# Kernel optimization log

Hardware: AMD Instinct MI355X
Metric: run time of the kernel (lower is better)

The kernel has to match this reference:

```python
import jax, jax.numpy as jnp
import numpy as np

NUM_REGIONS = 64
K_NEIGHBORS = 5
REGION_LAMBDA = 0.02
SPATIAL_LAMBDA = 0.0005


def setup_inputs() -> dict:
    key = jax.random.key(0)
    k1, k2, k3 = jax.random.split(key, 3)
    B = 16384
    c_points = jax.random.normal(k1, (B, 3), dtype=jnp.float32)
    coords_std = jax.random.normal(k2, (B, 3), dtype=jnp.float32)
    region_ids = jax.random.randint(k3, (B,), 0, NUM_REGIONS, dtype=jnp.int32)
    return {"c_points": c_points, "coords_std": coords_std, "region_ids": region_ids}


def _region_loss(c_points, region_ids):
    # Equivalent to per-region pairwise dispersion via segment reductions:
    # 2 * sum||c - mean_r||^2 / (max(n_r*(n_r-1)/2, 1) * xdim), summed over regions.
    dtype = c_points.dtype
    xdim = jnp.asarray(c_points.shape[1], dtype)
    ones = jnp.ones(c_points.shape[0], dtype)
    counts = jax.ops.segment_sum(ones, region_ids, num_segments=NUM_REGIONS)          # [R]
    sums = jax.ops.segment_sum(c_points, region_ids, num_segments=NUM_REGIONS)        # [R,3]
    sqs = jax.ops.segment_sum(c_points * c_points, region_ids, num_segments=NUM_REGIONS)  # [R,3]
    safe_n = jnp.maximum(counts, 1.0)
    mean = sums / safe_n[:, None]
    sum_sq_centered = jnp.sum(sqs - counts[:, None] * mean * mean, axis=1)             # [R]
    n_pairs = counts * (counts - 1.0) * 0.5
    denom = jnp.maximum(n_pairs, 1.0) * xdim
    per_region = jnp.where(counts > 1.0, 2.0 * sum_sq_centered / denom, 0.0)
    return jnp.asarray(REGION_LAMBDA, dtype) * jnp.sum(per_region)


def _spatial_loss(c_points, coords_std):
    # Dense pairwise squared distances, exclude self, KNN gather, mean squared diff of cuts.
    dtype = c_points.dtype
    B = coords_std.shape[0]
    xdim = jnp.asarray(c_points.shape[1], dtype)
    c2 = jnp.sum(coords_std * coords_std, axis=1, keepdims=True)                       # [B,1]
    d2 = c2 - 2.0 * (coords_std @ coords_std.T) + c2.T                                 # [B,B]
    big = jnp.max(d2) + 1.0
    diag = jnp.arange(B)
    d2 = d2.at[diag, diag].set(big)
    _, idxs = jax.lax.top_k(-d2, K_NEIGHBORS)                                          # [B,k]
    c_nb = c_points[idxs]                                                              # [B,k,3]
    diffs = c_points[:, None, :] - c_nb
    sq = jnp.sum(diffs * diffs, axis=2)                                                # [B,k]
    loss = jnp.mean(jnp.mean(sq, axis=1))
    return jnp.asarray(SPATIAL_LAMBDA, dtype) * (loss / jnp.maximum(xdim, 1.0))


def reference(c_points, coords_std, region_ids):
    return _region_loss(c_points, region_ids) + _spatial_loss(c_points, coords_std)
```

## Files before the change

kernel.cpp:

```cpp
#include <hip/hip_runtime.h>
#include <stdint.h>

#define B_N    16384
#define NREG   64
#define KNB    5
#define SAMPLE 4096
#define NSUB   16
#define SUBLEN (SAMPLE / NSUB)
#define NCH    32
#define CHLEN  (B_N / NCH)
#define MRGBLK 256
#define SENT   0xFFFF

static __device__ __forceinline__ float inf32() { return __int_as_float(0x7f800000); }
static __device__ __forceinline__ float med3(float a, float b, float c) {
    return __builtin_amdgcn_fmed3f(a, b, c);
}

#define MINS5(nv)                      \
    {                                  \
        s4 = med3(s3, s4, (nv));       \
        s3 = med3(s2, s3, (nv));       \
        s2 = med3(s1, s2, (nv));       \
        s1 = med3(s0, s1, (nv));       \
        s0 = fminf(s0, (nv));          \
    }

#define INS5(nv, jj)                                                        \
    {                                                                       \
        bool c4 = (nv) < s4, c3 = (nv) < s3, c2 = (nv) < s2,                \
             c1 = (nv) < s1, c0 = (nv) < s0;                                \
        s4 = c3 ? s3 : (c4 ? (nv) : s4);  i4 = c3 ? i3 : (c4 ? (jj) : i4);  \
        s3 = c2 ? s2 : (c3 ? (nv) : s3);  i3 = c2 ? i2 : (c3 ? (jj) : i3);  \
        s2 = c1 ? s1 : (c2 ? (nv) : s2);  i2 = c1 ? i1 : (c2 ? (jj) : i2);  \
        s1 = c0 ? s0 : (c1 ? (nv) : s1);  i1 = c0 ? i0 : (c1 ? (jj) : i1);  \
        s0 = c0 ? (nv) : s0;              i0 = c0 ? (jj) : i0;              \
    }

__global__ __launch_bounds__(256) void prep_kernel(const float* __restrict__ c,
                                                   const float* __restrict__ x,
                                                   const int* __restrict__ ids,
                                                   float4* __restrict__ pre,
                                                   float* __restrict__ wsreg,
                                                   int* __restrict__ counter) {
    const int blk = blockIdx.x;
    const int tid = threadIdx.x;
    if (blk < 64) {
        if (blk == 0 && tid == 0) *counter = 0;
        int j = blk * 256 + tid;
        float jx = x[3 * j + 0], jy = x[3 * j + 1], jz = x[3 * j + 2];
        pre[j] = make_float4(-2.f * jx, -2.f * jy, -2.f * jz,
                             jx * jx + jy * jy + jz * jz);
        return;
    }
    const int r = blk - 64;
    float cnt = 0.f, sx = 0.f, sy = 0.f, sz = 0.f, sxx = 0.f, syy = 0.f, szz = 0.f;
    for (int i = tid; i < B_N; i += 256) {
        int id = ids[i];
        float m = (id == r) ? 1.0f : 0.0f;
        float px = c[3 * i + 0], py = c[3 * i + 1], pz = c[3 * i + 2];
        cnt += m;
        sx += m * px;  sy += m * py;  sz += m * pz;
        sxx += m * px * px;  syy += m * py * py;  szz += m * pz * pz;
    }
    for (int off = 32; off > 0; off >>= 1) {
        cnt += __shfl_down(cnt, off);
        sx  += __shfl_down(sx, off);
        sy  += __shfl_down(sy, off);
        sz  += __shfl_down(sz, off);
        sxx += __shfl_down(sxx, off);
        syy += __shfl_down(syy, off);
        szz += __shfl_down(szz, off);
    }
    __shared__ float sb[4][7];
    const int lane = tid & 63, w = tid >> 6;
    if (lane == 0) {
        sb[w][0] = cnt; sb[w][1] = sx; sb[w][2] = sy; sb[w][3] = sz;
        sb[w][4] = sxx; sb[w][5] = syy; sb[w][6] = szz;
    }
    __syncthreads();
    if (tid == 0) {
        float C = 0, SX = 0, SY = 0, SZ = 0, SXX = 0, SYY = 0, SZZ = 0;
        for (int i = 0; i < 4; i++) {
            C += sb[i][0]; SX += sb[i][1]; SY += sb[i][2]; SZ += sb[i][3];
            SXX += sb[i][4]; SYY += sb[i][5]; SZZ += sb[i][6];
        }
        float safe = fmaxf(C, 1.0f);
        float mx = SX / safe, my = SY / safe, mz = SZ / safe;
        float ssc = (SXX - C * mx * mx) + (SYY - C * my * my) + (SZZ - C * mz * mz);
        float npairs = C * (C - 1.0f) * 0.5f;
        float denom = fmaxf(npairs, 1.0f) * 3.0f;
        wsreg[r] = (C > 1.0f) ? (2.0f * ssc / denom) : 0.0f;
    }
}

__global__ __launch_bounds__(256) void tau_scan_kernel(const float4* __restrict__ pre,
                                                       float* __restrict__ tauv) {
    __shared__ float4 tile[SUBLEN];
    const int tid = threadIdx.x;
    const int qb = blockIdx.x & 63;
    const int sub = blockIdx.x >> 6;
    const int q = qb * 256 + tid;
    const int j0 = sub * SUBLEN;

    tile[tid] = pre[j0 + tid];
    const float4 pq = pre[q];
    const float qx = -0.5f * pq.x, qy = -0.5f * pq.y, qz = -0.5f * pq.z;
    __syncthreads();

    float s0 = inf32(), s1 = inf32(), s2 = inf32(), s3 = inf32(), s4 = inf32();

    for (int jb = 0; jb < SUBLEN; jb += 8) {
        float dt[8];
#pragma unroll
        for (int u = 0; u < 8; ++u) {
            float4 pj = tile[jb + u];
            dt[u] = fmaf(pj.x, qx, fmaf(pj.y, qy, fmaf(pj.z, qz, pj.w)));
        }
#pragma unroll
        for (int u = 0; u < 8; ++u) {
            float nv = ((j0 + jb + u) != q) ? dt[u] : inf32();
            MINS5(nv);
        }
    }
    tauv[(sub * 5 + 0) * B_N + q] = s0;
    tauv[(sub * 5 + 1) * B_N + q] = s1;
    tauv[(sub * 5 + 2) * B_N + q] = s2;
    tauv[(sub * 5 + 3) * B_N + q] = s3;
    tauv[(sub * 5 + 4) * B_N + q] = s4;
}

__global__ __launch_bounds__(256) void tau_merge_kernel(const float* __restrict__ tauv,
                                                        float* __restrict__ tau) {
    const int q = blockIdx.x * 256 + threadIdx.x;
    float s0 = inf32(), s1 = inf32(), s2 = inf32(), s3 = inf32(), s4 = inf32();
#pragma unroll 8
    for (int n = 0; n < NSUB * 5; ++n) {
        float v = tauv[n * B_N + q];
        MINS5(v);
    }
    int b = __float_as_int(s4);
    b += (b >= 0) ? 1 : -1;
    tau[q] = __int_as_float(b);
}

__global__ __launch_bounds__(256) void spatial_kernel(const float4* __restrict__ pre,
                                                      const float* __restrict__ tau,
                                                      unsigned short* __restrict__ cand) {
    __shared__ float4 tile[CHLEN];
    const int tid = threadIdx.x;
    const int qb = blockIdx.x & 63;
    const int ch = blockIdx.x >> 6;
    const int q = qb * 256 + tid;
    const int jbase = ch * CHLEN;

#pragma unroll
    for (int i = 0; i < CHLEN / 256; ++i)
        tile[tid + i * 256] = pre[jbase + tid + i * 256];

    const float4 pq = pre[q];
    const float qx = -0.5f * pq.x, qy = -0.5f * pq.y, qz = -0.5f * pq.z;
    const float t = tau[q];
    __syncthreads();

    float s0 = t, s1 = t, s2 = t, s3 = t, s4 = t;
    int i0 = SENT, i1 = SENT, i2 = SENT, i3 = SENT, i4 = SENT;

    for (int jb = 0; jb < CHLEN; jb += 8) {
        float dt[8];
#pragma unroll
        for (int u = 0; u < 8; ++u) {
            float4 pj = tile[jb + u];
            dt[u] = fmaf(pj.x, qx, fmaf(pj.y, qy, fmaf(pj.z, qz, pj.w)));
        }
#pragma unroll
        for (int u = 0; u < 8; ++u) {
            if (__any(dt[u] < s4)) {
                int j = jbase + jb + u;
                bool p = (dt[u] < s4) && (j != q);
                float nv = p ? dt[u] : inf32();
                INS5(nv, j);
            }
        }
    }
    cand[(ch * 5 + 0) * B_N + q] = (unsigned short)i0;
    cand[(ch * 5 + 1) * B_N + q] = (unsigned short)i1;
    cand[(ch * 5 + 2) * B_N + q] = (unsigned short)i2;
    cand[(ch * 5 + 3) * B_N + q] = (unsigned short)i3;
    cand[(ch * 5 + 4) * B_N + q] = (unsigned short)i4;
}

__global__ __launch_bounds__(256) void merge_kernel(const float* __restrict__ c,
                                                    const float4* __restrict__ pre,
                                                    const unsigned short* __restrict__ cand,
                                                    const float* __restrict__ wsreg,
                                                    float* __restrict__ spart,
                                                    int* __restrict__ counter,
                                                    float* __restrict__ out) {
    const int tid = threadIdx.x;
    const int blk = blockIdx.x;
    const int qloc = tid >> 2;
    const int part = tid & 3;
    const int q = blk * 64 + qloc;
    const float4 pq = pre[q];
    const float qx = -0.5f * pq.x, qy = -0.5f * pq.y, qz = -0.5f * pq.z;

    __shared__ float dm[64][4][5];
    __shared__ unsigned short im[64][4][5];

    {
        float s0 = inf32(), s1 = inf32(), s2 = inf32(), s3 = inf32(), s4 = inf32();
        int i0 = SENT & 0x3FFF, i1 = i0, i2 = i0, i3 = i0, i4 = i0;
        const int n0 = part * (NCH / 4) * 5;
#pragma unroll 8
        for (int n = n0; n < n0 + (NCH / 4) * 5; ++n) {
            int cd = (int)cand[n * B_N + q];
            int safe = cd & 0x3FFF;
            float4 pj = pre[safe];
            float d = fmaf(pj.x, qx, fmaf(pj.y, qy, fmaf(pj.z, qz, pj.w)));
            float nv = (cd != SENT) ? d : inf32();
            INS5(nv, safe);
        }
        dm[qloc][part][0] = s0; im[qloc][part][0] = (unsigned short)i0;
        dm[qloc][part][1] = s1; im[qloc][part][1] = (unsigned short)i1;
        dm[qloc][part][2] = s2; im[qloc][part][2] = (unsigned short)i2;
        dm[qloc][part][3] = s3; im[qloc][part][3] = (unsigned short)i3;
        dm[qloc][part][4] = s4; im[qloc][part][4] = (unsigned short)i4;
    }
    __syncthreads();

    float acc = 0.f;
    if (part == 0) {
        float s0 = inf32(), s1 = inf32(), s2 = inf32(), s3 = inf32(), s4 = inf32();
        int i0 = 0, i1 = 0, i2 = 0, i3 = 0, i4 = 0;
#pragma unroll
        for (int p = 0; p < 4; ++p)
#pragma unroll
            for (int k = 0; k < 5; ++k) {
                float nv = dm[qloc][p][k];
                int jj = (int)im[qloc][p][k];
                INS5(nv, jj);
            }
        const float cx = c[3 * q + 0], cy = c[3 * q + 1], cz = c[3 * q + 2];
        int ks[5] = {i0, i1, i2, i3, i4};
#pragma unroll
        for (int n = 0; n < KNB; ++n) {
            int nb = ks[n];
            float dx = cx - c[3 * nb + 0];
            float dy = cy - c[3 * nb + 1];
            float dz = cz - c[3 * nb + 2];
            acc += dx * dx + dy * dy + dz * dz;
        }
    }
    acc += __shfl_down(acc, 32);
    acc += __shfl_down(acc, 16);
    acc += __shfl_down(acc, 8);
    acc += __shfl_down(acc, 4);
    __shared__ float wsum[4];
    __shared__ int last;
    const int lane = tid & 63, w = tid >> 6;
    if (lane == 0) wsum[w] = acc;
    __syncthreads();
    if (tid == 0) {
        float bs = wsum[0] + wsum[1] + wsum[2] + wsum[3];
        atomicExch(&spart[blk], bs);
        __threadfence();
        int old = atomicAdd(counter, 1);
        last = (old == MRGBLK - 1);
    }
    __syncthreads();
    if (last) {
        float s = atomicAdd(&spart[tid], 0.0f);
        float r = (tid < NREG) ? wsreg[tid] : 0.f;
        for (int off = 32; off > 0; off >>= 1) {
            s += __shfl_down(s, off);
            r += __shfl_down(r, off);
        }
        __shared__ float fb[4];
        if (lane == 0) fb[w] = s;
        __syncthreads();
        if (tid == 0) {
            float S = fb[0] + fb[1] + fb[2] + fb[3];
            float spatial_mean = S / (float)(B_N * KNB);
            out[0] = 0.02f * r + 0.0005f * (spatial_mean / 3.0f);
        }
    }
}

extern "C" void kernel_launch(void* const* d_in, const int* in_sizes, int n_in,
                              void* d_out, int out_size, void* d_ws, size_t ws_size,
                              hipStream_t stream) {
    const float* c  = (const float*)d_in[0];
    const float* x  = (const float*)d_in[1];
    const int* ids  = (const int*)d_in[2];
    float* out = (float*)d_out;

    char* ws = (char*)d_ws;
    float4* pre = (float4*)ws;
    float* tauv = (float*)(ws + (size_t)B_N * 16);
    unsigned short* cand =
        (unsigned short*)((char*)tauv + (size_t)NSUB * 5 * B_N * 4);
    float* tau = (float*)((char*)cand + (size_t)NCH * 5 * B_N * 2);
    float* wsreg = tau + B_N;
    float* spart = wsreg + NREG;
    int* counter = (int*)(spart + MRGBLK);

    hipLaunchKernelGGL(prep_kernel, dim3(128), dim3(256), 0, stream, c, x, ids, pre, wsreg, counter);
    hipLaunchKernelGGL(tau_scan_kernel, dim3(64 * NSUB), dim3(256), 0, stream, pre, tauv);
    hipLaunchKernelGGL(tau_merge_kernel, dim3(64), dim3(256), 0, stream, tauv, tau);
    hipLaunchKernelGGL(spatial_kernel, dim3(64 * NCH), dim3(256), 0, stream, pre, tau, cand);
    hipLaunchKernelGGL(merge_kernel, dim3(MRGBLK), dim3(256), 0, stream, c, pre, cand, wsreg, spart, counter, out);
}
```

Measured before the change: 107.1 us.

## Fuse prep and tau scan kernels, add batched early-reject in spatial scan

The prep kernel (pre-transform plus region sums) is merged into the tau scan kernel as 64 extra blocks. Scan blocks now compute their tile from raw coordinates instead of reading the precomputed buffer, so one launch and one dependency are gone. The spatial scan also takes the minimum of each group of 8 distances and skips the per-element insertion checks when no lane has a candidate below its threshold. The cost is some duplicated transform arithmetic and a larger, mixed-role grid.

```diff
diff --git a/kernel.cpp b/kernel.cpp
--- a/kernel.cpp
+++ b/kernel.cpp
@@ -37,75 +37,78 @@
         s0 = c0 ? (nv) : s0;              i0 = c0 ? (jj) : i0;              \
     }
 
-__global__ __launch_bounds__(256) void prep_kernel(const float* __restrict__ c,
-                                                   const float* __restrict__ x,
-                                                   const int* __restrict__ ids,
-                                                   float4* __restrict__ pre,
-                                                   float* __restrict__ wsreg,
-                                                   int* __restrict__ counter) {
+__global__ __launch_bounds__(256) void scan_region_kernel(const float* __restrict__ c,
+                                                          const float* __restrict__ x,
+                                                          const int* __restrict__ ids,
+                                                          float4* __restrict__ pre,
+                                                          float* __restrict__ tauv,
+                                                          float* __restrict__ wsreg,
+                                                          int* __restrict__ counter) {
     const int blk = blockIdx.x;
     const int tid = threadIdx.x;
-    if (blk < 64) {
-        if (blk == 0 && tid == 0) *counter = 0;
-        int j = blk * 256 + tid;
-        float jx = x[3 * j + 0], jy = x[3 * j + 1], jz = x[3 * j + 2];
-        pre[j] = make_float4(-2.f * jx, -2.f * jy, -2.f * jz,
-                             jx * jx + jy * jy + jz * jz);
+
+    if (blk >= 1024) {
+        const int r = blk - 1024;
+        if (r == 0 && tid == 0) *counter = 0;
+        {
+            int j = r * 256 + tid;
+            float jx = x[3 * j + 0], jy = x[3 * j + 1], jz = x[3 * j + 2];
+            pre[j] = make_float4(-2.f * jx, -2.f * jy, -2.f * jz,
+                                 jx * jx + jy * jy + jz * jz);
+        }
+        float cnt = 0.f, sx = 0.f, sy = 0.f, sz = 0.f, sxx = 0.f, syy = 0.f, szz = 0.f;
+        for (int i = tid; i < B_N; i += 256) {
+            int id = ids[i];
+            float m = (id == r) ? 1.0f : 0.0f;
+            float px = c[3 * i + 0], py = c[3 * i + 1], pz = c[3 * i + 2];
+            cnt += m;
+            sx += m * px;  sy += m * py;  sz += m * pz;
+            sxx += m * px * px;  syy += m * py * py;  szz += m * pz * pz;
+        }
+        for (int off = 32; off > 0; off >>= 1) {
+            cnt += __shfl_down(cnt, off);
+            sx  += __shfl_down(sx, off);
+            sy  += __shfl_down(sy, off);
+            sz  += __shfl_down(sz, off);
+            sxx += __shfl_down(sxx, off);
+            syy += __shfl_down(syy, off);
+            szz += __shfl_down(szz, off);
+        }
+        __shared__ float sb[4][7];
+        const int lane = tid & 63, w = tid >> 6;
+        if (lane == 0) {
+            sb[w][0] = cnt; sb[w][1] = sx; sb[w][2] = sy; sb[w][3] = sz;
+            sb[w][4] = sxx; sb[w][5] = syy; sb[w][6] = szz;
+        }
+        __syncthreads();
+        if (tid == 0) {
+            float C = 0, SX = 0, SY = 0, SZ = 0, SXX = 0, SYY = 0, SZZ = 0;
+            for (int i = 0; i < 4; i++) {
+                C += sb[i][0]; SX += sb[i][1]; SY += sb[i][2]; SZ += sb[i][3];
+                SXX += sb[i][4]; SYY += sb[i][5]; SZZ += sb[i][6];
+            }
+            float safe = fmaxf(C, 1.0f);
+            float mx = SX / safe, my = SY / safe, mz = SZ / safe;
+            float ssc = (SXX - C * mx * mx) + (SYY - C * my * my) + (SZZ - C * mz * mz);
+            float npairs = C * (C - 1.0f) * 0.5f;
+            float denom = fmaxf(npairs, 1.0f) * 3.0f;
+            wsreg[r] = (C > 1.0f) ? (2.0f * ssc / denom) : 0.0f;
+        }
         return;
     }
-    const int r = blk - 64;
-    float cnt = 0.f, sx = 0.f, sy = 0.f, sz = 0.f, sxx = 0.f, syy = 0.f, szz = 0.f;
-    for (int i = tid; i < B_N; i += 256) {
-        int id = ids[i];
-        float m = (id == r) ? 1.0f : 0.0f;
-        float px = c[3 * i + 0], py = c[3 * i + 1], pz = c[3 * i + 2];
-        cnt += m;
-        sx += m * px;  sy += m * py;  sz += m * pz;
-        sxx += m * px * px;  syy += m * py * py;  szz += m * pz * pz;
-    }
-    for (int off = 32; off > 0; off >>= 1) {
-        cnt += __shfl_down(cnt, off);
-        sx  += __shfl_down(sx, off);
-        sy  += __shfl_down(sy, off);
-        sz  += __shfl_down(sz, off);
-        sxx += __shfl_down(sxx, off);
-        syy += __shfl_down(syy, off);
-        szz += __shfl_down(szz, off);
-    }
-    __shared__ float sb[4][7];
-    const int lane = tid & 63, w = tid >> 6;
-    if (lane == 0) {
-        sb[w][0] = cnt; sb[w][1] = sx; sb[w][2] = sy; sb[w][3] = sz;
-        sb[w][4] = sxx; sb[w][5] = syy; sb[w][6] = szz;
-    }
-    __syncthreads();
-    if (tid == 0) {
-        float C = 0, SX = 0, SY = 0, SZ = 0, SXX = 0, SYY = 0, SZZ = 0;
-        for (int i = 0; i < 4; i++) {
-            C += sb[i][0]; SX += sb[i][1]; SY += sb[i][2]; SZ += sb[i][3];
-            SXX += sb[i][4]; SYY += sb[i][5]; SZZ += sb[i][6];
-        }
-        float safe = fmaxf(C, 1.0f);
-        float mx = SX / safe, my = SY / safe, mz = SZ / safe;
-        float ssc = (SXX - C * mx * mx) + (SYY - C * my * my) + (SZZ - C * mz * mz);
-        float npairs = C * (C - 1.0f) * 0.5f;
-        float denom = fmaxf(npairs, 1.0f) * 3.0f;
-        wsreg[r] = (C > 1.0f) ? (2.0f * ssc / denom) : 0.0f;
-    }
-}
-
-__global__ __launch_bounds__(256) void tau_scan_kernel(const float4* __restrict__ pre,
-                                                       float* __restrict__ tauv) {
+
     __shared__ float4 tile[SUBLEN];
-    const int tid = threadIdx.x;
-    const int qb = blockIdx.x & 63;
-    const int sub = blockIdx.x >> 6;
+    const int qb = blk & 63;
+    const int sub = blk >> 6;
     const int q = qb * 256 + tid;
     const int j0 = sub * SUBLEN;
-
-    tile[tid] = pre[j0 + tid];
-    const float4 pq = pre[q];
-    const float qx = -0.5f * pq.x, qy = -0.5f * pq.y, qz = -0.5f * pq.z;
+    {
+        int j = j0 + tid;
+        float jx = x[3 * j + 0], jy = x[3 * j + 1], jz = x[3 * j + 2];
+        tile[tid] = make_float4(-2.f * jx, -2.f * jy, -2.f * jz,
+                                jx * jx + jy * jy + jz * jz);
+    }
+    const float qx = x[3 * q + 0], qy = x[3 * q + 1], qz = x[3 * q + 2];
     __syncthreads();
 
     float s0 = inf32(), s1 = inf32(), s2 = inf32(), s3 = inf32(), s4 = inf32();
@@ -173,13 +176,17 @@
             float4 pj = tile[jb + u];
             dt[u] = fmaf(pj.x, qx, fmaf(pj.y, qy, fmaf(pj.z, qz, pj.w)));
         }
-#pragma unroll
-        for (int u = 0; u < 8; ++u) {
-            if (__any(dt[u] < s4)) {
-                int j = jbase + jb + u;
-                bool p = (dt[u] < s4) && (j != q);
-                float nv = p ? dt[u] : inf32();
-                INS5(nv, j);
+        float m = fminf(fminf(fminf(dt[0], dt[1]), fminf(dt[2], dt[3])),
+                        fminf(fminf(dt[4], dt[5]), fminf(dt[6], dt[7])));
+        if (__builtin_expect(__any(m < s4), 0)) {
+#pragma unroll
+            for (int u = 0; u < 8; ++u) {
+                if (__any(dt[u] < s4)) {
+                    int j = jbase + jb + u;
+                    bool p = (dt[u] < s4) && (j != q);
+                    float nv = p ? dt[u] : inf32();
+                    INS5(nv, j);
+                }
             }
         }
     }
@@ -305,9 +312,10 @@
     float* spart = wsreg + NREG;
     int* counter = (int*)(spart + MRGBLK);
 
-    hipLaunchKernelGGL(prep_kernel, dim3(128), dim3(256), 0, stream, c, x, ids, pre, wsreg, counter);
-    hipLaunchKernelGGL(tau_scan_kernel, dim3(64 * NSUB), dim3(256), 0, stream, pre, tauv);
+    hipLaunchKernelGGL(scan_region_kernel, dim3(1088), dim3(256), 0, stream,
+                       c, x, ids, pre, tauv, wsreg, counter);
     hipLaunchKernelGGL(tau_merge_kernel, dim3(64), dim3(256), 0, stream, tauv, tau);
     hipLaunchKernelGGL(spatial_kernel, dim3(64 * NCH), dim3(256), 0, stream, pre, tau, cand);
-    hipLaunchKernelGGL(merge_kernel, dim3(MRGBLK), dim3(256), 0, stream, c, pre, cand, wsreg, spart, counter, out);
-}
+    hipLaunchKernelGGL(merge_kernel, dim3(MRGBLK), dim3(256), 0, stream, c, pre, cand,
+                       wsreg, spart, counter, out);
+}
```

Result: faster. 92.45 us (-13.7%).
